# Kernel optimization log

Measured on AMD Instinct MI355X. Metric: run time of the kernel, lower is better.

Reference implementation:

```python
import jax, jax.numpy as jnp
import numpy as np

N, E, D_IN, H, D_OUT = 50000, 1600000, 256, 128, 64


def setup_inputs() -> dict:
    key = jax.random.key(0)
    ks = jax.random.split(key, 8)
    x = jax.random.normal(ks[0], (N, D_IN), dtype=jnp.float32)
    edge_index = jax.random.randint(ks[1], (2, E), 0, N, dtype=jnp.int64)
    W1 = jax.random.normal(ks[2], (D_IN, H), dtype=jnp.float32) / np.float32(np.sqrt(D_IN))
    b1 = jnp.zeros((H,), jnp.float32)
    W2 = jax.random.normal(ks[3], (H, H), dtype=jnp.float32) / np.float32(np.sqrt(H))
    b2 = jnp.zeros((H,), jnp.float32)
    W3 = jax.random.normal(ks[4], (H, D_OUT), dtype=jnp.float32) / np.float32(np.sqrt(H))
    b3 = jnp.zeros((D_OUT,), jnp.float32)
    return {"x": x, "W1": W1, "b1": b1, "W2": W2, "b2": b2, "W3": W3, "b3": b3,
            "edge_index": edge_index}


def reference(x, W1, b1, W2, b2, W3, b3, edge_index):
    n = x.shape[0]
    # GCN: add self-loops, symmetric normalization D^{-1/2}(A+I)D^{-1/2}
    loop = jnp.arange(n, dtype=edge_index.dtype)
    src = jnp.concatenate([edge_index[0], loop])
    dst = jnp.concatenate([edge_index[1], loop])
    deg = jax.ops.segment_sum(jnp.ones_like(dst, x.dtype), dst, num_segments=n)
    dinv = jnp.where(deg > 0, jax.lax.rsqrt(deg), 0.0).astype(x.dtype)
    norm = dinv[src] * dinv[dst]  # [E+N]

    def gcn_layer(h, W, b):
        h = h @ W                                   # [N, F_out]
        msg = norm[:, None] * h[src]                # gather + scale, [E+N, F_out]
        return jax.ops.segment_sum(msg, dst, num_segments=n) + b

    h = jax.nn.relu(gcn_layer(x, W1, b1))
    h = jax.nn.relu(gcn_layer(h, W2, b2))
    return gcn_layer(h, W3, b3)
```

## Files before the change

kernel.cpp:

```cpp
#include <hip/hip_runtime.h>


constexpr int DIN = 256;
constexpr int HID = 128;
constexpr int DOUT = 64;

typedef unsigned short ushort_t;
typedef unsigned int uint_t;
typedef __attribute__((ext_vector_type(8))) short bf16x8;
typedef __attribute__((ext_vector_type(4))) float f32x4;

__device__ inline ushort_t f2bf(float f) {
  uint_t u = __float_as_uint(f);
  u += 0x7FFF + ((u >> 16) & 1);
  return (ushort_t)(u >> 16);
}
__device__ inline float bf2f(ushort_t b) {
  return __uint_as_float(((uint_t)b) << 16);
}


__device__ inline void wprep_one(const float* __restrict__ W, ushort_t* __restrict__ Bhi,
                                 ushort_t* __restrict__ Blo, int K, int F, int i) {
  int k = i / F, nn = i % F;
  int t = nn >> 4, s = k >> 5, q = (k >> 3) & 3, j = k & 7;
  int lane = q * 16 + (nn & 15);
  int KS = K >> 5;
  size_t idx = (((size_t)t * KS + s) * 64 + (size_t)lane) * 8 + j;
  float w = W[i];
  ushort_t h = f2bf(w);
  float r = w - bf2f(h);
  Bhi[idx] = h;
  Blo[idx] = f2bf(r);
}


__global__ __launch_bounds__(256) void initprep_kernel(
    int* __restrict__ c0, int* __restrict__ c1, int* __restrict__ c2,
    int* __restrict__ c3, int n, int iblocks,
    const float* __restrict__ W1, ushort_t* __restrict__ W1hi, ushort_t* __restrict__ W1lo,
    const float* __restrict__ W2, ushort_t* __restrict__ W2hi, ushort_t* __restrict__ W2lo,
    const float* __restrict__ W3, ushort_t* __restrict__ W3hi, ushort_t* __restrict__ W3lo) {
  if ((int)blockIdx.x < iblocks) {
    int i = blockIdx.x * 256 + threadIdx.x;
    if (i < n) { c0[i] = 1; c1[i] = 0; c2[i] = 0; c3[i] = 0; }
  } else {
    int idx = ((int)blockIdx.x - iblocks) * 256 + threadIdx.x;
    constexpr int S1 = DIN * HID;
    constexpr int S2 = S1 + HID * HID;
    constexpr int S3 = S2 + HID * DOUT;
    if (idx < S1) wprep_one(W1, W1hi, W1lo, DIN, HID, idx);
    else if (idx < S2) wprep_one(W2, W2hi, W2lo, HID, HID, idx - S1);
    else if (idx < S3) wprep_one(W3, W3hi, W3lo, HID, DOUT, idx - S2);
  }
}


template <int K, int F, bool SCALE>
__device__ inline void gemm_mfma_dev(const float* __restrict__ X,
    const ushort_t* __restrict__ Bhi, const ushort_t* __restrict__ Blo,
    const float* __restrict__ dinv, ushort_t* __restrict__ T, int n, int bid) {
  constexpr int NT = F / 16;
  constexpr int KS = K / 32;
  int wave = threadIdx.x >> 6;
  int lane = threadIdx.x & 63;
  int q = lane >> 4;
  int m = lane & 15;
  int arow = bid * 64 + wave * 16 + m;
  bool valid = arow < n;
  const float* xrow = X + (size_t)arow * K;

  f32x4 acc[NT];
#pragma unroll
  for (int t = 0; t < NT; ++t) acc[t] = (f32x4){0.f, 0.f, 0.f, 0.f};

  for (int s = 0; s < KS; ++s) {
    float av[8];
    if (valid) {
      float4 u0 = *(const float4*)(xrow + s * 32 + q * 8);
      float4 u1 = *(const float4*)(xrow + s * 32 + q * 8 + 4);
      av[0] = u0.x; av[1] = u0.y; av[2] = u0.z; av[3] = u0.w;
      av[4] = u1.x; av[5] = u1.y; av[6] = u1.z; av[7] = u1.w;
    } else {
#pragma unroll
      for (int j = 0; j < 8; ++j) av[j] = 0.f;
    }
    bf16x8 ahi, alo;
#pragma unroll
    for (int j = 0; j < 8; ++j) {
      ushort_t h = f2bf(av[j]);
      ahi[j] = (short)h;
      alo[j] = (short)f2bf(av[j] - bf2f(h));
    }
#pragma unroll
    for (int t = 0; t < NT; ++t) {
      size_t boff = (((size_t)t * KS + s) * 64 + (size_t)lane) * 8;
      bf16x8 bh = *(const bf16x8*)(Bhi + boff);
      bf16x8 bl = *(const bf16x8*)(Blo + boff);
      acc[t] = __builtin_amdgcn_mfma_f32_16x16x32_bf16(ahi, bh, acc[t], 0, 0, 0);
      acc[t] = __builtin_amdgcn_mfma_f32_16x16x32_bf16(alo, bh, acc[t], 0, 0, 0);
      acc[t] = __builtin_amdgcn_mfma_f32_16x16x32_bf16(ahi, bl, acc[t], 0, 0, 0);
    }
  }

  int orow_base = bid * 64 + wave * 16 + q * 4;
#pragma unroll
  for (int r = 0; r < 4; ++r) {
    int orow = orow_base + r;
    if (orow >= n) continue;
    float sc = SCALE ? dinv[orow] : 1.0f;
    ushort_t* trow = T + (size_t)orow * F + m;
#pragma unroll
    for (int t = 0; t < NT; ++t) trow[t * 16] = f2bf(sc * acc[t][r]);
  }
}

template <int K, int F>
__global__ __launch_bounds__(256) void gemm_mfma_kernel(const float* __restrict__ X,
    const ushort_t* __restrict__ Bhi, const ushort_t* __restrict__ Blo,
    const float* __restrict__ dinv, ushort_t* __restrict__ T, int n) {
  gemm_mfma_dev<K, F, true>(X, Bhi, Blo, dinv, T, n, blockIdx.x);
}


__global__ __launch_bounds__(256) void fusedA_kernel(
    const float* __restrict__ X, const ushort_t* __restrict__ Bhi,
    const ushort_t* __restrict__ Blo, ushort_t* __restrict__ T, int n, int gblocks,
    const int* __restrict__ dst, int* __restrict__ c0, int* __restrict__ c1,
    int* __restrict__ c2, int* __restrict__ c3, int* __restrict__ slot, int e) {
  if ((int)blockIdx.x < gblocks) {
    gemm_mfma_dev<DIN, HID, false>(X, Bhi, Blo, nullptr, T, n, blockIdx.x);
  } else {
    int i = ((int)blockIdx.x - gblocks) * 256 + threadIdx.x;
    if (i >= e) return;
    int d = dst[i];
    int k = i & 3;
    int s;
    if      (k == 0) s = atomicAdd(&c0[d], 1);
    else if (k == 1) s = atomicAdd(&c1[d], 1);
    else if (k == 2) s = atomicAdd(&c2[d], 1);
    else             s = atomicAdd(&c3[d], 1);
    slot[i] = s;
  }
}


__global__ __launch_bounds__(256) void scanA_kernel(const int* __restrict__ c0,
    const int* __restrict__ c1, const int* __restrict__ c2, const int* __restrict__ c3,
    int* __restrict__ blocksum, int n) {
  __shared__ int sums[256];
  int t = threadIdx.x;
  int base = blockIdx.x * 1024 + t * 4;
  int local = 0;
#pragma unroll
  for (int k = 0; k < 4; ++k) {
    int i = base + k;
    if (i < n) local += c0[i] + c1[i] + c2[i] + c3[i] - 1;
  }
  sums[t] = local;
  __syncthreads();
  for (int off = 128; off > 0; off >>= 1) {
    if (t < off) sums[t] += sums[t + off];
    __syncthreads();
  }
  if (t == 0) blocksum[blockIdx.x] = sums[0];
}

__global__ __launch_bounds__(64) void scanB_kernel(int* __restrict__ blocksum, int nb) {
  int lane = threadIdx.x;
  int carry = 0;
  for (int base = 0; base < nb; base += 64) {
    int i = base + lane;
    int orig = (i < nb) ? blocksum[i] : 0;
    int v = orig;
#pragma unroll
    for (int off = 1; off < 64; off <<= 1) {
      int u = __shfl_up(v, off, 64);
      if (lane >= off) v += u;
    }
    int total = __shfl(v, 63, 64);
    if (i < nb) blocksum[i] = carry + v - orig;
    carry += total;
  }
}

__global__ __launch_bounds__(256) void scanC_kernel(const int* __restrict__ c0,
    const int* __restrict__ c1, const int* __restrict__ c2, const int* __restrict__ c3,
    const int* __restrict__ blocksum, int* __restrict__ row_start, int* __restrict__ deg,
    float* __restrict__ dinv, int4* __restrict__ sub, int n) {
  __shared__ int sums[256];
  int t = threadIdx.x;
  int base = blockIdx.x * 1024 + t * 4;
  int d[4], k0[4], k1[4], k2[4];
  int local = 0;
#pragma unroll
  for (int k = 0; k < 4; ++k) {
    int i = base + k;
    if (i < n) {
      k0[k] = c0[i]; k1[k] = c1[i]; k2[k] = c2[i];
      d[k] = k0[k] + k1[k] + k2[k] + c3[i];
      local += d[k] - 1;
    } else { d[k] = 1; k0[k] = 1; k1[k] = 0; k2[k] = 0; }
  }
  sums[t] = local;
  __syncthreads();
  for (int off = 1; off < 256; off <<= 1) {
    int v = (t >= off) ? sums[t - off] : 0;
    __syncthreads();
    sums[t] += v;
    __syncthreads();
  }
  int run = blocksum[blockIdx.x] + sums[t] - local;
#pragma unroll
  for (int k = 0; k < 4; ++k) {
    int i = base + k;
    if (i < n) {
      row_start[i] = run;
      deg[i] = d[k];
      dinv[i] = rsqrtf((float)d[k]);
      int4 sb;
      sb.x = run - 1;
      sb.y = run + (k0[k] - 1);
      sb.z = sb.y + k1[k];
      sb.w = sb.z + k2[k];
      sub[i] = sb;
      run += d[k] - 1;
    }
  }
}


__global__ __launch_bounds__(256) void fusedB_kernel(
    const int* __restrict__ src, const int* __restrict__ dst,
    const int* __restrict__ slot, const int4* __restrict__ sub,
    int* __restrict__ col, int e, int fblocks,
    ushort_t* __restrict__ T, const float* __restrict__ dinv, int n) {
  if ((int)blockIdx.x < fblocks) {
    int i = blockIdx.x * 256 + threadIdx.x;
    if (i >= e) return;
    int d = dst[i];
    int k = i & 3;
    int4 sb = sub[d];
    int base = (k == 0) ? sb.x : (k == 1) ? sb.y : (k == 2) ? sb.z : sb.w;
    col[base + slot[i]] = src[i];
  } else {
    int idx = ((int)blockIdx.x - fblocks) * 256 + threadIdx.x;
    int total = n * (HID / 8);
    if (idx >= total) return;
    int row = idx >> 4;
    float sc = dinv[row];
    uint4* p = (uint4*)T + idx;
    uint4 v = *p;
    uint_t w[4] = {v.x, v.y, v.z, v.w};
#pragma unroll
    for (int j = 0; j < 4; ++j) {
      float lo = sc * bf2f((ushort_t)(w[j] & 0xFFFF));
      float hi = sc * bf2f((ushort_t)(w[j] >> 16));
      w[j] = (uint_t)f2bf(lo) | ((uint_t)f2bf(hi) << 16);
    }
    v.x = w[0]; v.y = w[1]; v.z = w[2]; v.w = w[3];
    *p = v;
  }
}


template <int F, bool RELU>
__global__ __launch_bounds__(256) void spmm_kernel(const ushort_t* __restrict__ t,
    const int* __restrict__ row_start, const int* __restrict__ deg,
    const int* __restrict__ col, const float* __restrict__ dinv,
    const float* __restrict__ bias, float* __restrict__ out, int n) {
  int gw = (int)((blockIdx.x * 256u + threadIdx.x) >> 6);
  int lane = threadIdx.x & 63;
  int n0 = gw * 2;
  int n1 = n0 + 1;
  if (n0 >= n) return;
  bool h1 = (n1 < n);
  int rs0 = row_start[n0], e0 = deg[n0] - 1;
  int rs1 = h1 ? row_start[n1] : 0, e1 = h1 ? (deg[n1] - 1) : 0;
  float di0 = dinv[n0];
  float di1 = h1 ? dinv[n1] : 0.f;

  if constexpr (F == 128) {
    uint_t s0 = ((const uint_t*)(t + (size_t)n0 * F))[lane];
    float ax0 = bf2f((ushort_t)(s0 & 0xFFFF)), ay0 = bf2f((ushort_t)(s0 >> 16));
    float ax1 = 0.f, ay1 = 0.f;
    if (h1) {
      uint_t s1 = ((const uint_t*)(t + (size_t)n1 * F))[lane];
      ax1 = bf2f((ushort_t)(s1 & 0xFFFF)); ay1 = bf2f((ushort_t)(s1 >> 16));
    }
    int p0 = rs0, q0 = rs0 + e0;
    int p1 = rs1, q1 = rs1 + e1;
    while (p0 + 4 <= q0 && p1 + 4 <= q1) {
      int c[8];
      uint_t v[8];
#pragma unroll
      for (int j = 0; j < 4; ++j) { c[j] = col[p0 + j]; c[4 + j] = col[p1 + j]; }
#pragma unroll
      for (int j = 0; j < 8; ++j) v[j] = ((const uint_t*)(t + (size_t)c[j] * F))[lane];
#pragma unroll
      for (int j = 0; j < 4; ++j) {
        ax0 += bf2f((ushort_t)(v[j] & 0xFFFF));
        ay0 += bf2f((ushort_t)(v[j] >> 16));
        ax1 += bf2f((ushort_t)(v[4 + j] & 0xFFFF));
        ay1 += bf2f((ushort_t)(v[4 + j] >> 16));
      }
      p0 += 4; p1 += 4;
    }
    for (; p0 + 4 <= q0; p0 += 4) {
      int c[4]; uint_t v[4];
#pragma unroll
      for (int j = 0; j < 4; ++j) c[j] = col[p0 + j];
#pragma unroll
      for (int j = 0; j < 4; ++j) v[j] = ((const uint_t*)(t + (size_t)c[j] * F))[lane];
#pragma unroll
      for (int j = 0; j < 4; ++j) {
        ax0 += bf2f((ushort_t)(v[j] & 0xFFFF)); ay0 += bf2f((ushort_t)(v[j] >> 16));
      }
    }
    for (; p0 < q0; ++p0) {
      uint_t v = ((const uint_t*)(t + (size_t)col[p0] * F))[lane];
      ax0 += bf2f((ushort_t)(v & 0xFFFF)); ay0 += bf2f((ushort_t)(v >> 16));
    }
    for (; p1 + 4 <= q1; p1 += 4) {
      int c[4]; uint_t v[4];
#pragma unroll
      for (int j = 0; j < 4; ++j) c[j] = col[p1 + j];
#pragma unroll
      for (int j = 0; j < 4; ++j) v[j] = ((const uint_t*)(t + (size_t)c[j] * F))[lane];
#pragma unroll
      for (int j = 0; j < 4; ++j) {
        ax1 += bf2f((ushort_t)(v[j] & 0xFFFF)); ay1 += bf2f((ushort_t)(v[j] >> 16));
      }
    }
    for (; p1 < q1; ++p1) {
      uint_t v = ((const uint_t*)(t + (size_t)col[p1] * F))[lane];
      ax1 += bf2f((ushort_t)(v & 0xFFFF)); ay1 += bf2f((ushort_t)(v >> 16));
    }
    float bx = bias[2 * lane], by = bias[2 * lane + 1];
    ax0 = fmaf(di0, ax0, bx); ay0 = fmaf(di0, ay0, by);
    if constexpr (RELU) { ax0 = fmaxf(ax0, 0.f); ay0 = fmaxf(ay0, 0.f); }
    float2 o0; o0.x = ax0; o0.y = ay0;
    ((float2*)(out + (size_t)n0 * F))[lane] = o0;
    if (h1) {
      ax1 = fmaf(di1, ax1, bx); ay1 = fmaf(di1, ay1, by);
      if constexpr (RELU) { ax1 = fmaxf(ax1, 0.f); ay1 = fmaxf(ay1, 0.f); }
      float2 o1; o1.x = ax1; o1.y = ay1;
      ((float2*)(out + (size_t)n1 * F))[lane] = o1;
    }
  } else {
    float a0 = bf2f(t[(size_t)n0 * F + lane]);
    float a1 = h1 ? bf2f(t[(size_t)n1 * F + lane]) : 0.f;
    int p0 = rs0, q0 = rs0 + e0;
    int p1 = rs1, q1 = rs1 + e1;
    while (p0 + 4 <= q0 && p1 + 4 <= q1) {
      int c[8];
      ushort_t v[8];
#pragma unroll
      for (int j = 0; j < 4; ++j) { c[j] = col[p0 + j]; c[4 + j] = col[p1 + j]; }
#pragma unroll
      for (int j = 0; j < 8; ++j) v[j] = t[(size_t)c[j] * F + lane];
#pragma unroll
      for (int j = 0; j < 4; ++j) { a0 += bf2f(v[j]); a1 += bf2f(v[4 + j]); }
      p0 += 4; p1 += 4;
    }
    for (; p0 + 4 <= q0; p0 += 4) {
      int c[4]; ushort_t v[4];
#pragma unroll
      for (int j = 0; j < 4; ++j) c[j] = col[p0 + j];
#pragma unroll
      for (int j = 0; j < 4; ++j) v[j] = t[(size_t)c[j] * F + lane];
#pragma unroll
      for (int j = 0; j < 4; ++j) a0 += bf2f(v[j]);
    }
    for (; p0 < q0; ++p0) a0 += bf2f(t[(size_t)col[p0] * F + lane]);
    for (; p1 + 4 <= q1; p1 += 4) {
      int c[4]; ushort_t v[4];
#pragma unroll
      for (int j = 0; j < 4; ++j) c[j] = col[p1 + j];
#pragma unroll
      for (int j = 0; j < 4; ++j) v[j] = t[(size_t)c[j] * F + lane];
#pragma unroll
      for (int j = 0; j < 4; ++j) a1 += bf2f(v[j]);
    }
    for (; p1 < q1; ++p1) a1 += bf2f(t[(size_t)col[p1] * F + lane]);
    float b = bias[lane];
    a0 = fmaf(di0, a0, b);
    if constexpr (RELU) a0 = fmaxf(a0, 0.f);
    out[(size_t)n0 * F + lane] = a0;
    if (h1) {
      a1 = fmaf(di1, a1, b);
      if constexpr (RELU) a1 = fmaxf(a1, 0.f);
      out[(size_t)n1 * F + lane] = a1;
    }
  }
}


extern "C" void kernel_launch(void* const* d_in, const int* in_sizes, int n_in,
                              void* d_out, int out_size, void* d_ws, size_t ws_size,
                              hipStream_t stream) {
  const float* x  = (const float*)d_in[0];
  const float* W1 = (const float*)d_in[1];
  const float* b1 = (const float*)d_in[2];
  const float* W2 = (const float*)d_in[3];
  const float* b2 = (const float*)d_in[4];
  const float* W3 = (const float*)d_in[5];
  const float* b3 = (const float*)d_in[6];
  const int* ei   = (const int*)d_in[7];

  int n = in_sizes[0] / DIN;
  int e = in_sizes[7] / 2;
  const int* src = ei;
  const int* dst = ei + e;

  char* ws = (char*)d_ws;
  size_t off = 0;
  auto alloc = [&](size_t bytes) -> void* {
    off = (off + 255) & ~(size_t)255;
    void* p = ws + off;
    off += bytes;
    return p;
  };
  int nscan = (n + 1023) / 1024;
  int*      c0        = (int*)alloc((size_t)n * 4);
  int*      c1        = (int*)alloc((size_t)n * 4);
  int*      c2        = (int*)alloc((size_t)n * 4);
  int*      c3        = (int*)alloc((size_t)n * 4);
  int*      deg       = (int*)alloc((size_t)n * 4);
  float*    dinv      = (float*)alloc((size_t)n * 4);
  int*      row_start = (int*)alloc((size_t)n * 4);
  int4*     sub       = (int4*)alloc((size_t)n * 16);
  int*      blocksum  = (int*)alloc((size_t)nscan * 4);
  int*      slot      = (int*)alloc((size_t)e * 4);
  int*      col       = (int*)alloc((size_t)e * 4);
  ushort_t* T         = (ushort_t*)alloc((size_t)n * HID * 2);
  float*    Hf        = (float*)alloc((size_t)n * HID * 4);
  ushort_t* W1hi      = (ushort_t*)alloc((size_t)DIN * HID * 2);
  ushort_t* W1lo      = (ushort_t*)alloc((size_t)DIN * HID * 2);
  ushort_t* W2hi      = (ushort_t*)alloc((size_t)HID * HID * 2);
  ushort_t* W2lo      = (ushort_t*)alloc((size_t)HID * HID * 2);
  ushort_t* W3hi      = (ushort_t*)alloc((size_t)HID * DOUT * 2);
  ushort_t* W3lo      = (ushort_t*)alloc((size_t)HID * DOUT * 2);
  (void)ws_size;

  int nb256 = (n + 255) / 256;
  int eb256 = (e + 255) / 256;
  int gemm_blocks = (n + 63) / 64;
  int nwaves = (n + 1) / 2;
  int spmm_blocks = (nwaves + 3) / 4;
  constexpr int WPREP_TOTAL = DIN * HID + HID * HID + HID * DOUT;
  int wblocks = (WPREP_TOTAL + 255) / 256;
  int sblocks = (n * (HID / 8) + 255) / 256;

  initprep_kernel<<<nb256 + wblocks, 256, 0, stream>>>(
      c0, c1, c2, c3, n, nb256,
      W1, W1hi, W1lo, W2, W2hi, W2lo, W3, W3hi, W3lo);
  fusedA_kernel<<<gemm_blocks + eb256, 256, 0, stream>>>(
      x, W1hi, W1lo, T, n, gemm_blocks,
      dst, c0, c1, c2, c3, slot, e);
  scanA_kernel<<<nscan, 256, 0, stream>>>(c0, c1, c2, c3, blocksum, n);
  scanB_kernel<<<1, 64, 0, stream>>>(blocksum, nscan);
  scanC_kernel<<<nscan, 256, 0, stream>>>(c0, c1, c2, c3, blocksum, row_start, deg, dinv, sub, n);
  fusedB_kernel<<<eb256 + sblocks, 256, 0, stream>>>(
      src, dst, slot, sub, col, e, eb256, T, dinv, n);

  spmm_kernel<HID, true><<<spmm_blocks, 256, 0, stream>>>(T, row_start, deg, col, dinv, b1, Hf, n);
  gemm_mfma_kernel<HID, HID><<<gemm_blocks, 256, 0, stream>>>(Hf, W2hi, W2lo, dinv, T, n);
  spmm_kernel<HID, true><<<spmm_blocks, 256, 0, stream>>>(T, row_start, deg, col, dinv, b2, Hf, n);
  gemm_mfma_kernel<HID, DOUT><<<gemm_blocks, 256, 0, stream>>>(Hf, W3hi, W3lo, dinv, T, n);
  spmm_kernel<DOUT, false><<<spmm_blocks, 256, 0, stream>>>(T, row_start, deg, col, dinv, b3, (float*)d_out, n);
}
```

Measured before the change: 404.6 us.

## Replace global atomic CSR build with per-block LDS histograms and column scan

```diff
diff --git a/kernel.cpp b/kernel.cpp
--- a/kernel.cpp
+++ b/kernel.cpp
@@ -4,6 +4,8 @@
 constexpr int DIN = 256;
 constexpr int HID = 128;
 constexpr int DOUT = 64;
+constexpr int NBLK = 64;
+constexpr int SLICE = 12544;
 
 typedef unsigned short ushort_t;
 typedef unsigned int uint_t;
@@ -34,25 +36,17 @@
   Blo[idx] = f2bf(r);
 }
 
-
-__global__ __launch_bounds__(256) void initprep_kernel(
-    int* __restrict__ c0, int* __restrict__ c1, int* __restrict__ c2,
-    int* __restrict__ c3, int n, int iblocks,
+__global__ __launch_bounds__(256) void wprep_kernel(
     const float* __restrict__ W1, ushort_t* __restrict__ W1hi, ushort_t* __restrict__ W1lo,
     const float* __restrict__ W2, ushort_t* __restrict__ W2hi, ushort_t* __restrict__ W2lo,
     const float* __restrict__ W3, ushort_t* __restrict__ W3hi, ushort_t* __restrict__ W3lo) {
-  if ((int)blockIdx.x < iblocks) {
-    int i = blockIdx.x * 256 + threadIdx.x;
-    if (i < n) { c0[i] = 1; c1[i] = 0; c2[i] = 0; c3[i] = 0; }
-  } else {
-    int idx = ((int)blockIdx.x - iblocks) * 256 + threadIdx.x;
-    constexpr int S1 = DIN * HID;
-    constexpr int S2 = S1 + HID * HID;
-    constexpr int S3 = S2 + HID * DOUT;
-    if (idx < S1) wprep_one(W1, W1hi, W1lo, DIN, HID, idx);
-    else if (idx < S2) wprep_one(W2, W2hi, W2lo, HID, HID, idx - S1);
-    else if (idx < S3) wprep_one(W3, W3hi, W3lo, HID, DOUT, idx - S2);
-  }
+  int idx = blockIdx.x * 256 + threadIdx.x;
+  constexpr int S1 = DIN * HID;
+  constexpr int S2 = S1 + HID * HID;
+  constexpr int S3 = S2 + HID * DOUT;
+  if (idx < S1) wprep_one(W1, W1hi, W1lo, DIN, HID, idx);
+  else if (idx < S2) wprep_one(W2, W2hi, W2lo, HID, HID, idx - S1);
+  else if (idx < S3) wprep_one(W3, W3hi, W3lo, HID, DOUT, idx - S2);
 }
 
 
@@ -123,30 +117,55 @@
 }
 
 
-__global__ __launch_bounds__(256) void fusedA_kernel(
+__global__ __launch_bounds__(256) void fusedH_kernel(
+    const int* __restrict__ dst, int* __restrict__ blockhist,
+    int* __restrict__ lslot, int e, int chunk, int n,
     const float* __restrict__ X, const ushort_t* __restrict__ Bhi,
-    const ushort_t* __restrict__ Blo, ushort_t* __restrict__ T, int n, int gblocks,
-    const int* __restrict__ dst, int* __restrict__ c0, int* __restrict__ c1,
-    int* __restrict__ c2, int* __restrict__ c3, int* __restrict__ slot, int e) {
-  if ((int)blockIdx.x < gblocks) {
-    gemm_mfma_dev<DIN, HID, false>(X, Bhi, Blo, nullptr, T, n, blockIdx.x);
+    const ushort_t* __restrict__ Blo, ushort_t* __restrict__ T, int nn) {
+  __shared__ int h[SLICE];
+  if ((int)blockIdx.x < NBLK) {
+    int b = blockIdx.x;
+    int i0 = b * chunk;
+    int i1 = i0 + chunk; if (i1 > e) i1 = e;
+#pragma unroll 1
+    for (int s = 0; s < 4; ++s) {
+      int base = s * SLICE;
+      for (int j = threadIdx.x; j < SLICE; j += 256) h[j] = 0;
+      __syncthreads();
+      for (int i = i0 + threadIdx.x; i < i1; i += 256) {
+        int r = dst[i] - base;
+        if (r >= 0 && r < SLICE) lslot[i] = atomicAdd(&h[r], 1);
+      }
+      __syncthreads();
+      for (int j = threadIdx.x; j < SLICE; j += 256) {
+        int bin = base + j;
+        if (bin < n) blockhist[(size_t)b * n + bin] = h[j];
+      }
+      __syncthreads();
+    }
   } else {
-    int i = ((int)blockIdx.x - gblocks) * 256 + threadIdx.x;
-    if (i >= e) return;
-    int d = dst[i];
-    int k = i & 3;
-    int s;
-    if      (k == 0) s = atomicAdd(&c0[d], 1);
-    else if (k == 1) s = atomicAdd(&c1[d], 1);
-    else if (k == 2) s = atomicAdd(&c2[d], 1);
-    else             s = atomicAdd(&c3[d], 1);
-    slot[i] = s;
-  }
-}
-
-
-__global__ __launch_bounds__(256) void scanA_kernel(const int* __restrict__ c0,
-    const int* __restrict__ c1, const int* __restrict__ c2, const int* __restrict__ c3,
+    gemm_mfma_dev<DIN, HID, false>(X, Bhi, Blo, nullptr, T, nn, (int)blockIdx.x - NBLK);
+  }
+}
+
+
+__global__ __launch_bounds__(256) void colscan_kernel(int* __restrict__ blockhist,
+    int* __restrict__ cnt, int n) {
+  int d = blockIdx.x * 256 + threadIdx.x;
+  if (d >= n) return;
+  int run = 0;
+#pragma unroll 4
+  for (int b = 0; b < NBLK; ++b) {
+    size_t idx = (size_t)b * n + d;
+    int c = blockhist[idx];
+    blockhist[idx] = run;
+    run += c;
+  }
+  cnt[d] = run;
+}
+
+
+__global__ __launch_bounds__(256) void scanA_kernel(const int* __restrict__ cnt,
     int* __restrict__ blocksum, int n) {
   __shared__ int sums[256];
   int t = threadIdx.x;
@@ -155,7 +174,7 @@
 #pragma unroll
   for (int k = 0; k < 4; ++k) {
     int i = base + k;
-    if (i < n) local += c0[i] + c1[i] + c2[i] + c3[i] - 1;
+    if (i < n) local += cnt[i];
   }
   sums[t] = local;
   __syncthreads();
@@ -184,23 +203,19 @@
   }
 }
 
-__global__ __launch_bounds__(256) void scanC_kernel(const int* __restrict__ c0,
-    const int* __restrict__ c1, const int* __restrict__ c2, const int* __restrict__ c3,
-    const int* __restrict__ blocksum, int* __restrict__ row_start, int* __restrict__ deg,
-    float* __restrict__ dinv, int4* __restrict__ sub, int n) {
+__global__ __launch_bounds__(256) void scanC_kernel(const int* __restrict__ cnt,
+    const int* __restrict__ blocksum, int* __restrict__ row_start,
+    float* __restrict__ dinv, int n) {
   __shared__ int sums[256];
   int t = threadIdx.x;
   int base = blockIdx.x * 1024 + t * 4;
-  int d[4], k0[4], k1[4], k2[4];
+  int c[4];
   int local = 0;
 #pragma unroll
   for (int k = 0; k < 4; ++k) {
     int i = base + k;
-    if (i < n) {
-      k0[k] = c0[i]; k1[k] = c1[i]; k2[k] = c2[i];
-      d[k] = k0[k] + k1[k] + k2[k] + c3[i];
-      local += d[k] - 1;
-    } else { d[k] = 1; k0[k] = 1; k1[k] = 0; k2[k] = 0; }
+    c[k] = (i < n) ? cnt[i] : 0;
+    local += c[k];
   }
   sums[t] = local;
   __syncthreads();
@@ -216,15 +231,8 @@
     int i = base + k;
     if (i < n) {
       row_start[i] = run;
-      deg[i] = d[k];
-      dinv[i] = rsqrtf((float)d[k]);
-      int4 sb;
-      sb.x = run - 1;
-      sb.y = run + (k0[k] - 1);
-      sb.z = sb.y + k1[k];
-      sb.w = sb.z + k2[k];
-      sub[i] = sb;
-      run += d[k] - 1;
+      dinv[i] = rsqrtf((float)(c[k] + 1));
+      run += c[k];
     }
   }
 }
@@ -232,17 +240,17 @@
 
 __global__ __launch_bounds__(256) void fusedB_kernel(
     const int* __restrict__ src, const int* __restrict__ dst,
-    const int* __restrict__ slot, const int4* __restrict__ sub,
-    int* __restrict__ col, int e, int fblocks,
+    const int* __restrict__ lslot, const int* __restrict__ blockhist,
+    const int* __restrict__ row_start, int* __restrict__ col,
+    int e, int chunk, int fblocks,
     ushort_t* __restrict__ T, const float* __restrict__ dinv, int n) {
   if ((int)blockIdx.x < fblocks) {
     int i = blockIdx.x * 256 + threadIdx.x;
     if (i >= e) return;
     int d = dst[i];
-    int k = i & 3;
-    int4 sb = sub[d];
-    int base = (k == 0) ? sb.x : (k == 1) ? sb.y : (k == 2) ? sb.z : sb.w;
-    col[base + slot[i]] = src[i];
+    int b = i / chunk;
+    int pos = row_start[d] + blockhist[(size_t)b * n + d] + lslot[i];
+    col[pos] = src[i];
   } else {
     int idx = ((int)blockIdx.x - fblocks) * 256 + threadIdx.x;
     int total = n * (HID / 8);
@@ -266,7 +274,7 @@
 
 template <int F, bool RELU>
 __global__ __launch_bounds__(256) void spmm_kernel(const ushort_t* __restrict__ t,
-    const int* __restrict__ row_start, const int* __restrict__ deg,
+    const int* __restrict__ row_start, const int* __restrict__ cntArr,
     const int* __restrict__ col, const float* __restrict__ dinv,
     const float* __restrict__ bias, float* __restrict__ out, int n) {
   int gw = (int)((blockIdx.x * 256u + threadIdx.x) >> 6);
@@ -275,8 +283,10 @@
   int n1 = n0 + 1;
   if (n0 >= n) return;
   bool h1 = (n1 < n);
-  int rs0 = row_start[n0], e0 = deg[n0] - 1;
-  int rs1 = h1 ? row_start[n1] : 0, e1 = h1 ? (deg[n1] - 1) : 0;
+  int rs0 = __builtin_amdgcn_readfirstlane(row_start[n0]);
+  int e0 = __builtin_amdgcn_readfirstlane(cntArr[n0]);
+  int rs1 = h1 ? __builtin_amdgcn_readfirstlane(row_start[n1]) : 0;
+  int e1 = h1 ? __builtin_amdgcn_readfirstlane(cntArr[n1]) : 0;
   float di0 = dinv[n0];
   float di1 = h1 ? dinv[n1] : 0.f;
 
@@ -412,6 +422,7 @@
   int e = in_sizes[7] / 2;
   const int* src = ei;
   const int* dst = ei + e;
+  int chunk = (e + NBLK - 1) / NBLK;
 
   char* ws = (char*)d_ws;
   size_t off = 0;
@@ -422,16 +433,12 @@
     return p;
   };
   int nscan = (n + 1023) / 1024;
-  int*      c0        = (int*)alloc((size_t)n * 4);
-  int*      c1        = (int*)alloc((size_t)n * 4);
-  int*      c2        = (int*)alloc((size_t)n * 4);
-  int*      c3        = (int*)alloc((size_t)n * 4);
-  int*      deg       = (int*)alloc((size_t)n * 4);
+  int*      blockhist = (int*)alloc((size_t)NBLK * n * 4);
+  int*      lslot     = (int*)alloc((size_t)e * 4);
+  int*      cnt       = (int*)alloc((size_t)n * 4);
   float*    dinv      = (float*)alloc((size_t)n * 4);
   int*      row_start = (int*)alloc((size_t)n * 4);
-  int4*     sub       = (int4*)alloc((size_t)n * 16);
   int*      blocksum  = (int*)alloc((size_t)nscan * 4);
-  int*      slot      = (int*)alloc((size_t)e * 4);
   int*      col       = (int*)alloc((size_t)e * 4);
   ushort_t* T         = (ushort_t*)alloc((size_t)n * HID * 2);
   float*    Hf        = (float*)alloc((size_t)n * HID * 4);
@@ -443,7 +450,6 @@
   ushort_t* W3lo      = (ushort_t*)alloc((size_t)HID * DOUT * 2);
   (void)ws_size;
 
-  int nb256 = (n + 255) / 256;
   int eb256 = (e + 255) / 256;
   int gemm_blocks = (n + 63) / 64;
   int nwaves = (n + 1) / 2;
@@ -452,21 +458,21 @@
   int wblocks = (WPREP_TOTAL + 255) / 256;
   int sblocks = (n * (HID / 8) + 255) / 256;
 
-  initprep_kernel<<<nb256 + wblocks, 256, 0, stream>>>(
-      c0, c1, c2, c3, n, nb256,
+  wprep_kernel<<<wblocks, 256, 0, stream>>>(
       W1, W1hi, W1lo, W2, W2hi, W2lo, W3, W3hi, W3lo);
-  fusedA_kernel<<<gemm_blocks + eb256, 256, 0, stream>>>(
-      x, W1hi, W1lo, T, n, gemm_blocks,
-      dst, c0, c1, c2, c3, slot, e);
-  scanA_kernel<<<nscan, 256, 0, stream>>>(c0, c1, c2, c3, blocksum, n);
+  fusedH_kernel<<<NBLK + gemm_blocks, 256, 0, stream>>>(
+      dst, blockhist, lslot, e, chunk, n,
+      x, W1hi, W1lo, T, n);
+  colscan_kernel<<<(n + 255) / 256, 256, 0, stream>>>(blockhist, cnt, n);
+  scanA_kernel<<<nscan, 256, 0, stream>>>(cnt, blocksum, n);
   scanB_kernel<<<1, 64, 0, stream>>>(blocksum, nscan);
-  scanC_kernel<<<nscan, 256, 0, stream>>>(c0, c1, c2, c3, blocksum, row_start, deg, dinv, sub, n);
+  scanC_kernel<<<nscan, 256, 0, stream>>>(cnt, blocksum, row_start, dinv, n);
   fusedB_kernel<<<eb256 + sblocks, 256, 0, stream>>>(
-      src, dst, slot, sub, col, e, eb256, T, dinv, n);
-
-  spmm_kernel<HID, true><<<spmm_blocks, 256, 0, stream>>>(T, row_start, deg, col, dinv, b1, Hf, n);
+      src, dst, lslot, blockhist, row_start, col, e, chunk, eb256, T, dinv, n);
+
+  spmm_kernel<HID, true><<<spmm_blocks, 256, 0, stream>>>(T, row_start, cnt, col, dinv, b1, Hf, n);
   gemm_mfma_kernel<HID, HID><<<gemm_blocks, 256, 0, stream>>>(Hf, W2hi, W2lo, dinv, T, n);
-  spmm_kernel<HID, true><<<spmm_blocks, 256, 0, stream>>>(T, row_start, deg, col, dinv, b2, Hf, n);
+  spmm_kernel<HID, true><<<spmm_blocks, 256, 0, stream>>>(T, row_start, cnt, col, dinv, b2, Hf, n);
   gemm_mfma_kernel<HID, DOUT><<<gemm_blocks, 256, 0, stream>>>(Hf, W3hi, W3lo, dinv, T, n);
-  spmm_kernel<DOUT, false><<<spmm_blocks, 256, 0, stream>>>(T, row_start, deg, col, dinv, b3, (float*)d_out, n);
-}
+  spmm_kernel<DOUT, false><<<spmm_blocks, 256, 0, stream>>>(T, row_start, cnt, col, dinv, b3, (float*)d_out, n);
+}
```

New measurement: 477.5 us. +18.0%, slower.
